# Performance work log

Hardware: AMD Instinct MI355X
Metric: run time of the kernel (lower is better)

## Reference

```python
import jax, jax.numpy as jnp
import numpy as np

B, Q, K, D, H = 4, 2048, 2048, 512, 8
DH = D // H
MASK_VAL = -1e6


def setup_inputs() -> dict:
    key = jax.random.key(0)
    ks = jax.random.split(key, 8)
    queries = jax.random.normal(ks[0], (B, Q, D), dtype=jnp.float32)
    keys = jax.random.normal(ks[1], (B, K, D), dtype=jnp.float32)
    values = jax.random.normal(ks[2], (B, K, D), dtype=jnp.float32)
    valid_lens = jax.random.randint(ks[3], (B,), 1, K + 1, dtype=jnp.int32)
    # torch nn.Linear weights: shape [out_features, in_features], y = x @ W.T
    s = 1.0 / np.sqrt(D)
    W_q = jax.random.uniform(ks[4], (D, D), jnp.float32, -s, s)
    W_k = jax.random.uniform(ks[5], (D, D), jnp.float32, -s, s)
    W_v = jax.random.uniform(ks[6], (D, D), jnp.float32, -s, s)
    W_o = jax.random.uniform(ks[7], (D, D), jnp.float32, -s, s)
    return {"queries": queries, "keys": keys, "values": values,
            "valid_lens": valid_lens, "W_q": W_q, "W_k": W_k,
            "W_v": W_v, "W_o": W_o}


def _split_heads(x):
    # [B, S, D] -> [B, H, S, DH]
    b, s, _ = x.shape
    return x.reshape(b, s, H, DH).transpose(0, 2, 1, 3)


def reference(queries, keys, values, valid_lens, W_q, W_k, W_v, W_o):
    q = _split_heads(queries @ W_q.T)   # [B,H,Q,DH]
    k = _split_heads(keys @ W_k.T)      # [B,H,K,DH]
    v = _split_heads(values @ W_v.T)    # [B,H,K,DH]
    scores = jnp.einsum("bhqd,bhkd->bhqk", q, k) / jnp.sqrt(jnp.float32(DH))
    # padding mask: key position < valid_len[b], broadcast over heads & queries
    mask = jnp.arange(K)[None, None, None, :] < valid_lens[:, None, None, None]
    scores = jnp.where(mask, scores, MASK_VAL)
    attn = jax.nn.softmax(scores, axis=-1)  # dropout=eval/no-op
    out = jnp.einsum("bhqk,bhkd->bhqd", attn, v)
    out = out.transpose(0, 2, 1, 3).reshape(queries.shape[0], q.shape[2], D)
    return out @ W_o.T
```

## Files before the change

kernel.cpp:

```cpp
#include <hip/hip_runtime.h>
#include <cstdint>
#include <cstddef>

#define BB  4
#define QQ  2048
#define SK  2048
#define DD  512
#define HH  8
#define DHH 64
#define SPLIT 4

typedef __bf16 bf16;
typedef bf16  bf16x8 __attribute__((ext_vector_type(8)));
typedef bf16  bf16x4 __attribute__((ext_vector_type(4)));
typedef float f32x4  __attribute__((ext_vector_type(4)));
typedef _Float16 f16;
typedef f16   f16x4 __attribute__((ext_vector_type(4)));
typedef f16   f16x8 __attribute__((ext_vector_type(8)));

__device__ __forceinline__ void async16(void* lds, const void* g) {
  __builtin_amdgcn_global_load_lds(
      (const __attribute__((address_space(1))) unsigned int*)g,
      (__attribute__((address_space(3))) unsigned int*)lds, 16, 0, 0);
}

__global__ __launch_bounds__(256) void cvt_all(
    const float* __restrict__ q, const float* __restrict__ k,
    const float* __restrict__ v, const float* __restrict__ w0,
    const float* __restrict__ w1, const float* __restrict__ w2,
    const float* __restrict__ w3, bf16* __restrict__ dq,
    bf16* __restrict__ dk, bf16* __restrict__ dv, bf16* __restrict__ dw0,
    bf16* __restrict__ dw1, bf16* __restrict__ dw2, bf16* __restrict__ dw3,
    int nx4, int nw4) {
  const int y = blockIdx.y;
  const float* s;
  bf16* d;
  int n4;
  if (y < 3) {
    n4 = nx4; s = y == 0 ? q : y == 1 ? k : v;
    d = y == 0 ? dq : y == 1 ? dk : dv;
  } else {
    n4 = nw4;
    s = y == 3 ? w0 : y == 4 ? w1 : y == 5 ? w2 : w3;
    d = y == 3 ? dw0 : y == 4 ? dw1 : y == 5 ? dw2 : dw3;
  }
  int i = blockIdx.x * 256 + threadIdx.x;
  if (i < n4) {
    float4 vv = ((const float4*)s)[i];
    bf16x4 o;
    o[0] = (bf16)vv.x; o[1] = (bf16)vv.y; o[2] = (bf16)vv.z; o[3] = (bf16)vv.w;
    ((bf16x4*)d)[i] = o;
  }
}

template <typename EpiF>
__device__ __forceinline__ void gemm_body(
    const bf16* __restrict__ A, const bf16* __restrict__ Bt, EpiF epi_fn) {
  __shared__ __align__(16) bf16 lA[2][128 * 64];
  __shared__ __align__(16) bf16 lB[2][64 * 64];
  const int tid  = threadIdx.x;
  const int l    = tid & 63;
  const int w    = tid >> 6;
  const int lrow = l & 15, lq = l >> 4;
  const int wm = (w >> 1) * 64, wn = (w & 1) * 32;
  const int tM = blockIdx.y * 128, tN = blockIdx.x * 64;

  auto stage = [&](int kt, int buf) {
#pragma unroll
    for (int j = 0; j < 4; ++j) {
      int c = j * 256 + tid, row = c >> 3, gcc = (c & 7) ^ (row & 7);
      async16(&lA[buf][c * 8], &A[(size_t)(tM + row) * DD + kt + gcc * 8]);
    }
#pragma unroll
    for (int j = 0; j < 2; ++j) {
      int c = j * 256 + tid, row = c >> 3, gcc = (c & 7) ^ (row & 7);
      async16(&lB[buf][c * 8], &Bt[(size_t)(tN + row) * DD + kt + gcc * 8]);
    }
  };

  f32x4 acc[4][2] = {};
  stage(0, 0);
  for (int it = 0; it < 8; ++it) {
    __syncthreads();
    if (it + 1 < 8) stage((it + 1) * 64, (it + 1) & 1);
    const bf16* bufA = lA[it & 1];
    const bf16* bufB = lB[it & 1];
#pragma unroll
    for (int ks = 0; ks < 2; ++ks) {
      bf16x8 af[4], bfr[2];
#pragma unroll
      for (int mt = 0; mt < 4; ++mt) {
        int row = wm + mt * 16 + lrow;
        int chunk = row * 8 + ((ks * 4 + lq) ^ (lrow & 7));
        af[mt] = *(const bf16x8*)&bufA[chunk * 8];
      }
#pragma unroll
      for (int nt = 0; nt < 2; ++nt) {
        int row = wn + nt * 16 + lrow;
        int chunk = row * 8 + ((ks * 4 + lq) ^ (lrow & 7));
        bfr[nt] = *(const bf16x8*)&bufB[chunk * 8];
      }
#pragma unroll
      for (int mt = 0; mt < 4; ++mt)
#pragma unroll
        for (int nt = 0; nt < 2; ++nt)
          acc[mt][nt] = __builtin_amdgcn_mfma_f32_16x16x32_bf16(
              af[mt], bfr[nt], acc[mt][nt], 0, 0, 0);
    }
  }

#pragma unroll
  for (int mt = 0; mt < 4; ++mt)
#pragma unroll
    for (int nt = 0; nt < 2; ++nt) {
      int gi0 = tM + wm + mt * 16 + lq * 4;
      int gc  = tN + wn + nt * 16 + lrow;
      epi_fn(acc[mt][nt], gi0, gc);
    }
}

__global__ __launch_bounds__(256, 3) void proj3(
    const bf16* __restrict__ xq, const bf16* __restrict__ wq, bf16* __restrict__ qh,
    const bf16* __restrict__ xk, const bf16* __restrict__ wk, bf16* __restrict__ kh,
    const bf16* __restrict__ xv, const bf16* __restrict__ wv, bf16* __restrict__ vt,
    float qscale) {
  const int z = blockIdx.z;
  const bf16* A  = z == 0 ? xq : z == 1 ? xk : xv;
  const bf16* Bt = z == 0 ? wq : z == 1 ? wk : wv;
  bf16* Cout     = z == 0 ? qh : z == 1 ? kh : vt;
  const float scale = z == 0 ? qscale : 1.0f;
  gemm_body(A, Bt, [&](const f32x4& a, int gi0, int gc) {
    if (z == 2) {
      int b2 = gi0 >> 11, s0 = gi0 & 2047;
      int h2 = gc >> 6,  dh = gc & 63;
      int tile = s0 >> 6, kk = s0 & 63;
      int g = kk >> 4, a2 = (kk >> 2) & 3;
      int idx0 = ((g >> 1) * 4 + a2) * 8 + (g & 1) * 4;
      bf16x4 o;
#pragma unroll
      for (int r = 0; r < 4; ++r) o[r] = (bf16)a[r];
      *(bf16x4*)&Cout[((size_t)(b2 * HH + h2) * DHH + dh) * SK + tile * 64 + idx0] = o;
    } else {
#pragma unroll
      for (int r = 0; r < 4; ++r) {
        int gi = gi0 + r;
        int b2 = gi >> 11, s = gi & 2047;
        int h2 = gc >> 6,  dh = gc & 63;
        Cout[((size_t)(b2 * HH + h2) * QQ + s) * DHH + dh] = (bf16)(a[r] * scale);
      }
    }
  });
}

__global__ __launch_bounds__(256, 3) void proj_o(
    const bf16* __restrict__ A, const bf16* __restrict__ Bt,
    float* __restrict__ Cout) {
  gemm_body(A, Bt, [&](const f32x4& a, int gi0, int gc) {
#pragma unroll
    for (int r = 0; r < 4; ++r)
      Cout[(size_t)(gi0 + r) * DD + gc] = a[r];
  });
}

__global__ __launch_bounds__(256, 5) void attn_split(
    const bf16* __restrict__ qh, const bf16* __restrict__ kh,
    const bf16* __restrict__ vt, const int* __restrict__ valid_lens,
    f16* __restrict__ opart, float* __restrict__ lpart) {
  __shared__ __align__(16) bf16 lK[2][64 * 64];
  __shared__ __align__(16) bf16 lV[2][64 * 64];
  const int tid  = threadIdx.x;
  const int l    = tid & 63;
  const int w    = tid >> 6;
  const int lrow = l & 15, lq = l >> 4;
  const int rx   = lrow & 7;
  const int bh = blockIdx.x;
  const int b = bh >> 3;
  const int qt = blockIdx.y, z = blockIdx.z;
  const int vl  = valid_lens[b];
  const int nkt = (vl + 63) >> 6;
  const int chunk = (nkt + SPLIT - 1) / SPLIT;
  const int kt0 = z * chunk;
  const int kt1 = min(nkt, kt0 + chunk);
  const size_t pbase = ((size_t)bh * 32 + qt) * SPLIT + z;
  float* lout = lpart + pbase * 64;
  f16*   oout = opart + pbase * 4096;

  if (kt0 >= kt1) {
    if (lq == 0) lout[w * 16 + lrow] = 0.f;
    return;
  }

  const int q0 = qt * 64 + w * 16;
  const bf16* qbase = qh + (size_t)bh * QQ * DHH;
  const bf16* kbase = kh + (size_t)bh * SK * DHH;
  const bf16* vbase = vt + (size_t)bh * DHH * SK;

  bf16x8 qf[2];
#pragma unroll
  for (int ks = 0; ks < 2; ++ks)
    qf[ks] = *(const bf16x8*)&qbase[(size_t)(q0 + lrow) * DHH + ks * 32 + lq * 8];

  auto stageKV = [&](int k0, int buf) {
#pragma unroll
    for (int j = 0; j < 2; ++j) {
      int c = j * 256 + tid, row = c >> 3, gcc = (c & 7) ^ (row & 7);
      async16(&lK[buf][c * 8], &kbase[(size_t)(k0 + row) * DHH + gcc * 8]);
    }
#pragma unroll
    for (int j = 0; j < 2; ++j) {
      int c = j * 256 + tid, row = c >> 3, gcc = (c & 7) ^ (row & 7);
      async16(&lV[buf][c * 8], &vbase[(size_t)row * SK + k0 + gcc * 8]);
    }
  };

  f32x4 acc[4] = {};
  float rs = 0.f;

  stageKV(kt0 * 64, kt0 & 1);
  for (int kt = kt0; kt < kt1; ++kt) {
    __syncthreads();
    if (kt + 1 < kt1) stageKV((kt + 1) * 64, (kt + 1) & 1);
    const bf16* bufK = lK[kt & 1];
    const bf16* bufV = lV[kt & 1];
    const int k0 = kt * 64;

    f32x4 s[4] = {};
#pragma unroll
    for (int ks = 0; ks < 2; ++ks) {
#pragma unroll
      for (int t = 0; t < 4; ++t) {
        int row = t * 16 + lrow;
        int chunkc = row * 8 + ((ks * 4 + lq) ^ rx);
        bf16x8 kf = *(const bf16x8*)&bufK[chunkc * 8];
        s[t] = __builtin_amdgcn_mfma_f32_16x16x32_bf16(kf, qf[ks], s[t], 0, 0, 0);
      }
    }

    if (vl < k0 + 64) {
#pragma unroll
      for (int t = 0; t < 4; ++t) {
        int kb = k0 + t * 16 + lq * 4;
#pragma unroll
        for (int r = 0; r < 4; ++r)
          if (kb + r >= vl) s[t][r] = -1e30f;
      }
    }

    bf16x4 sb[4];
#pragma unroll
    for (int t = 0; t < 4; ++t)
#pragma unroll
      for (int r = 0; r < 4; ++r) {
        float p = __builtin_amdgcn_exp2f(fminf(s[t][r], 80.f));
        rs += p;
        sb[t][r] = (bf16)p;
      }

#pragma unroll
    for (int p = 0; p < 2; ++p) {
      bf16x8 pb;
#pragma unroll
      for (int r = 0; r < 4; ++r) { pb[r] = sb[2 * p][r]; pb[4 + r] = sb[2 * p + 1][r]; }
      int cc = (p * 4 + lq) ^ rx;
#pragma unroll
      for (int mt = 0; mt < 4; ++mt) {
        int row = mt * 16 + lrow;
        bf16x8 vf = *(const bf16x8*)&bufV[(row * 8 + cc) * 8];
        acc[mt] = __builtin_amdgcn_mfma_f32_16x16x32_bf16(vf, pb, acc[mt], 0, 0, 0);
      }
    }
  }

  rs += __shfl_xor(rs, 16);
  rs += __shfl_xor(rs, 32);
  if (lq == 0) lout[w * 16 + lrow] = rs;

#pragma unroll
  for (int mt = 0; mt < 4; ++mt) {
    f16x4 o;
#pragma unroll
    for (int r = 0; r < 4; ++r) o[r] = (f16)acc[mt][r];
    *(f16x4*)&oout[(w * 16 + lrow) * 64 + mt * 16 + lq * 4] = o;
  }
}

__global__ __launch_bounds__(256) void attn_combine(
    const f16* __restrict__ opart, const float* __restrict__ lpart,
    bf16* __restrict__ ao) {
  const int bh = blockIdx.x, qt = blockIdx.y;
  const int b = bh >> 3, h = bh & 7;
  const size_t base = ((size_t)bh * 32 + qt) * SPLIT;
  const int t = threadIdx.x, q = t >> 2, ds = (t & 3) * 16;
  float O[16] = {};
  float lsum = 0.f;
#pragma unroll
  for (int z = 0; z < SPLIT; ++z) {
    float lz = lpart[(base + z) * 64 + q];
    if (lz != 0.f) {
      lsum += lz;
      const f16x8* p = (const f16x8*)&opart[(base + z) * 4096 + q * 64 + ds];
      f16x8 a = p[0], c = p[1];
#pragma unroll
      for (int r = 0; r < 8; ++r) { O[r] += (float)a[r]; O[8 + r] += (float)c[r]; }
    }
  }
  float inv = 1.0f / lsum;
  bf16x8 o0, o1;
#pragma unroll
  for (int r = 0; r < 8; ++r) {
    o0[r] = (bf16)(O[r] * inv);
    o1[r] = (bf16)(O[8 + r] * inv);
  }
  bf16* dst = &ao[((size_t)(b * QQ + qt * 64 + q)) * DD + h * DHH + ds];
  *(bf16x8*)dst = o0;
  *(bf16x8*)(dst + 8) = o1;
}

extern "C" void kernel_launch(void* const* d_in, const int* in_sizes, int n_in,
                              void* d_out, int out_size, void* d_ws, size_t ws_size,
                              hipStream_t stream) {
  const float* queries    = (const float*)d_in[0];
  const float* keys       = (const float*)d_in[1];
  const float* values     = (const float*)d_in[2];
  const int*   valid_lens = (const int*)d_in[3];
  const float* W_q = (const float*)d_in[4];
  const float* W_k = (const float*)d_in[5];
  const float* W_v = (const float*)d_in[6];
  const float* W_o = (const float*)d_in[7];

  const size_t NX = (size_t)BB * QQ * DD;
  const size_t NW = (size_t)DD * DD;

  bf16* xq = (bf16*)d_ws;
  bf16* xk = xq + NX;
  bf16* xv = xk + NX;
  bf16* wq = xv + NX;
  bf16* wk = wq + NW;
  bf16* wv = wk + NW;
  bf16* wo = wv + NW;
  bf16* qh = wo + NW;
  bf16* kh = qh + NX;
  bf16* vt = kh + NX;
  f16*  opart = (f16*)(vt + NX);
  float* lpart = (float*)(opart + (size_t)32 * 32 * SPLIT * 4096);
  bf16* ao = xq;

  dim3 blk(256);
  cvt_all<<<dim3(NX / 1024, 7), blk, 0, stream>>>(
      queries, keys, values, W_q, W_k, W_v, W_o,
      xq, xk, xv, wq, wk, wv, wo, (int)(NX / 4), (int)(NW / 4));

  const float qscale = 0.125f * 1.44269504088896340736f;
  dim3 gg(DD / 64, (BB * QQ) / 128, 3);
  proj3<<<gg, blk, 0, stream>>>(xq, wq, qh, xk, wk, kh, xv, wv, vt, qscale);

  attn_split<<<dim3(BB * HH, QQ / 64, SPLIT), blk, 0, stream>>>(
      qh, kh, vt, valid_lens, opart, lpart);
  attn_combine<<<dim3(BB * HH, QQ / 64), blk, 0, stream>>>(opart, lpart, ao);

  proj_o<<<dim3(DD / 64, (BB * QQ) / 128), blk, 0, stream>>>(ao, wo, (float*)d_out);
}
```

Before: 202.9 us.

## Enlarge GEMM and attention tiles, fixed key chunks, transposed Q/K/O projections

```diff
diff --git a/kernel.cpp b/kernel.cpp
--- a/kernel.cpp
+++ b/kernel.cpp
@@ -8,7 +8,8 @@
 #define DD  512
 #define HH  8
 #define DHH 64
-#define SPLIT 4
+#define CS  8
+#define ZMAX 4
 
 typedef __bf16 bf16;
 typedef bf16  bf16x8 __attribute__((ext_vector_type(8)));
@@ -22,6 +23,11 @@
   __builtin_amdgcn_global_load_lds(
       (const __attribute__((address_space(1))) unsigned int*)g,
       (__attribute__((address_space(3))) unsigned int*)lds, 16, 0, 0);
+}
+
+__device__ __forceinline__ uint32_t pk2(float lo, float hi) {
+  return __builtin_amdgcn_perm(__builtin_bit_cast(uint32_t, hi),
+                               __builtin_bit_cast(uint32_t, lo), 0x07060302u);
 }
 
 __global__ __launch_bounds__(256) void cvt_all(
@@ -53,32 +59,32 @@
   }
 }
 
-template <typename EpiF>
+template <int MT, typename EpiF>
 __device__ __forceinline__ void gemm_body(
-    const bf16* __restrict__ A, const bf16* __restrict__ Bt, EpiF epi_fn) {
-  __shared__ __align__(16) bf16 lA[2][128 * 64];
-  __shared__ __align__(16) bf16 lB[2][64 * 64];
+    const bf16* __restrict__ A, const bf16* __restrict__ B,
+    int tM, int tN, EpiF epi_fn) {
+  __shared__ __align__(16) bf16 lA[2][MT * 32 * 64];
+  __shared__ __align__(16) bf16 lB[2][128 * 64];
   const int tid  = threadIdx.x;
   const int l    = tid & 63;
   const int w    = tid >> 6;
   const int lrow = l & 15, lq = l >> 4;
-  const int wm = (w >> 1) * 64, wn = (w & 1) * 32;
-  const int tM = blockIdx.y * 128, tN = blockIdx.x * 64;
+  const int wm = (w >> 1) * (MT * 16), wn = (w & 1) * 64;
 
   auto stage = [&](int kt, int buf) {
+#pragma unroll
+    for (int j = 0; j < MT; ++j) {
+      int c = j * 256 + tid, row = c >> 3, gcc = (c & 7) ^ (row & 7);
+      async16(&lA[buf][c * 8], &A[(size_t)(tM + row) * DD + kt + gcc * 8]);
+    }
 #pragma unroll
     for (int j = 0; j < 4; ++j) {
       int c = j * 256 + tid, row = c >> 3, gcc = (c & 7) ^ (row & 7);
-      async16(&lA[buf][c * 8], &A[(size_t)(tM + row) * DD + kt + gcc * 8]);
-    }
-#pragma unroll
-    for (int j = 0; j < 2; ++j) {
-      int c = j * 256 + tid, row = c >> 3, gcc = (c & 7) ^ (row & 7);
-      async16(&lB[buf][c * 8], &Bt[(size_t)(tN + row) * DD + kt + gcc * 8]);
+      async16(&lB[buf][c * 8], &B[(size_t)(tN + row) * DD + kt + gcc * 8]);
     }
   };
 
-  f32x4 acc[4][2] = {};
+  f32x4 acc[MT][4] = {};
   stage(0, 0);
   for (int it = 0; it < 8; ++it) {
     __syncthreads();
@@ -87,82 +93,85 @@
     const bf16* bufB = lB[it & 1];
 #pragma unroll
     for (int ks = 0; ks < 2; ++ks) {
-      bf16x8 af[4], bfr[2];
-#pragma unroll
-      for (int mt = 0; mt < 4; ++mt) {
+      bf16x8 af[MT], bfr[4];
+#pragma unroll
+      for (int mt = 0; mt < MT; ++mt) {
         int row = wm + mt * 16 + lrow;
         int chunk = row * 8 + ((ks * 4 + lq) ^ (lrow & 7));
         af[mt] = *(const bf16x8*)&bufA[chunk * 8];
       }
 #pragma unroll
-      for (int nt = 0; nt < 2; ++nt) {
+      for (int nt = 0; nt < 4; ++nt) {
         int row = wn + nt * 16 + lrow;
         int chunk = row * 8 + ((ks * 4 + lq) ^ (lrow & 7));
         bfr[nt] = *(const bf16x8*)&bufB[chunk * 8];
       }
 #pragma unroll
-      for (int mt = 0; mt < 4; ++mt)
-#pragma unroll
-        for (int nt = 0; nt < 2; ++nt)
+      for (int mt = 0; mt < MT; ++mt)
+#pragma unroll
+        for (int nt = 0; nt < 4; ++nt)
           acc[mt][nt] = __builtin_amdgcn_mfma_f32_16x16x32_bf16(
               af[mt], bfr[nt], acc[mt][nt], 0, 0, 0);
     }
   }
 
 #pragma unroll
-  for (int mt = 0; mt < 4; ++mt)
-#pragma unroll
-    for (int nt = 0; nt < 2; ++nt) {
-      int gi0 = tM + wm + mt * 16 + lq * 4;
-      int gc  = tN + wn + nt * 16 + lrow;
-      epi_fn(acc[mt][nt], gi0, gc);
-    }
-}
-
-__global__ __launch_bounds__(256, 3) void proj3(
+  for (int mt = 0; mt < MT; ++mt)
+#pragma unroll
+    for (int nt = 0; nt < 4; ++nt) {
+      int row0 = tM + wm + mt * 16 + lq * 4;
+      int col  = tN + wn + nt * 16 + lrow;
+      epi_fn(acc[mt][nt], row0, col);
+    }
+}
+
+__global__ __launch_bounds__(256, 2) void proj3(
     const bf16* __restrict__ xq, const bf16* __restrict__ wq, bf16* __restrict__ qh,
     const bf16* __restrict__ xk, const bf16* __restrict__ wk, bf16* __restrict__ kh,
     const bf16* __restrict__ xv, const bf16* __restrict__ wv, bf16* __restrict__ vt,
     float qscale) {
-  const int z = blockIdx.z;
-  const bf16* A  = z == 0 ? xq : z == 1 ? xk : xv;
-  const bf16* Bt = z == 0 ? wq : z == 1 ? wk : wv;
-  bf16* Cout     = z == 0 ? qh : z == 1 ? kh : vt;
-  const float scale = z == 0 ? qscale : 1.0f;
-  gemm_body(A, Bt, [&](const f32x4& a, int gi0, int gc) {
-    if (z == 2) {
-      int b2 = gi0 >> 11, s0 = gi0 & 2047;
-      int h2 = gc >> 6,  dh = gc & 63;
+  const int z = blockIdx.y, x = blockIdx.x;
+  if (z < 2) {
+    const bf16* A  = z == 0 ? wq : wk;
+    const bf16* B  = z == 0 ? xq : xk;
+    bf16* Cout     = z == 0 ? qh : kh;
+    const float scale = z == 0 ? qscale : 1.0f;
+    int tM = (x & 3) * 128, tN = (x >> 2) * 128;
+    gemm_body<4>(A, B, tM, tN, [&](const f32x4& a, int row0, int col) {
+      int b2 = col >> 11, s = col & 2047;
+      int h2 = row0 >> 6, dh0 = row0 & 63;
+      bf16x4 o;
+#pragma unroll
+      for (int r = 0; r < 4; ++r) o[r] = (bf16)(a[r] * scale);
+      *(bf16x4*)&Cout[((size_t)(b2 * HH + h2) * QQ + s) * DHH + dh0] = o;
+    });
+  } else {
+    int tM = (x >> 2) * 128, tN = (x & 3) * 128;
+    gemm_body<4>(xv, wv, tM, tN, [&](const f32x4& a, int row0, int col) {
+      int b2 = row0 >> 11, s0 = row0 & 2047;
+      int h2 = col >> 6,  dh = col & 63;
       int tile = s0 >> 6, kk = s0 & 63;
       int g = kk >> 4, a2 = (kk >> 2) & 3;
       int idx0 = ((g >> 1) * 4 + a2) * 8 + (g & 1) * 4;
       bf16x4 o;
 #pragma unroll
       for (int r = 0; r < 4; ++r) o[r] = (bf16)a[r];
-      *(bf16x4*)&Cout[((size_t)(b2 * HH + h2) * DHH + dh) * SK + tile * 64 + idx0] = o;
-    } else {
-#pragma unroll
-      for (int r = 0; r < 4; ++r) {
-        int gi = gi0 + r;
-        int b2 = gi >> 11, s = gi & 2047;
-        int h2 = gc >> 6,  dh = gc & 63;
-        Cout[((size_t)(b2 * HH + h2) * QQ + s) * DHH + dh] = (bf16)(a[r] * scale);
-      }
-    }
+      *(bf16x4*)&vt[((size_t)(b2 * HH + h2) * DHH + dh) * SK + tile * 64 + idx0] = o;
+    });
+  }
+}
+
+__global__ __launch_bounds__(256, 2) void proj_o(
+    const bf16* __restrict__ wo, const bf16* __restrict__ ao,
+    float* __restrict__ Cout) {
+  const int x = blockIdx.x;
+  int tM = (x & 7) * 64, tN = (x >> 3) * 128;
+  gemm_body<2>(wo, ao, tM, tN, [&](const f32x4& a, int row0, int col) {
+    *(float4*)&Cout[(size_t)col * DD + row0] = *(const float4*)&a;
   });
 }
 
-__global__ __launch_bounds__(256, 3) void proj_o(
-    const bf16* __restrict__ A, const bf16* __restrict__ Bt,
-    float* __restrict__ Cout) {
-  gemm_body(A, Bt, [&](const f32x4& a, int gi0, int gc) {
-#pragma unroll
-    for (int r = 0; r < 4; ++r)
-      Cout[(size_t)(gi0 + r) * DD + gc] = a[r];
-  });
-}
-
-__global__ __launch_bounds__(256, 5) void attn_split(
+__global__ __launch_bounds__(256, 4) void attn_split(
     const bf16* __restrict__ qh, const bf16* __restrict__ kh,
     const bf16* __restrict__ vt, const int* __restrict__ valid_lens,
     f16* __restrict__ opart, float* __restrict__ lpart) {
@@ -178,27 +187,29 @@
   const int qt = blockIdx.y, z = blockIdx.z;
   const int vl  = valid_lens[b];
   const int nkt = (vl + 63) >> 6;
-  const int chunk = (nkt + SPLIT - 1) / SPLIT;
-  const int kt0 = z * chunk;
-  const int kt1 = min(nkt, kt0 + chunk);
-  const size_t pbase = ((size_t)bh * 32 + qt) * SPLIT + z;
-  float* lout = lpart + pbase * 64;
-  f16*   oout = opart + pbase * 4096;
+  const int kt0 = z * CS;
+  const int kt1 = min(nkt, kt0 + CS);
+  const size_t pbase = ((size_t)bh * 16 + qt) * ZMAX + z;
+  float* lout = lpart + pbase * 128;
+  f16*   oout = opart + pbase * 8192;
 
   if (kt0 >= kt1) {
-    if (lq == 0) lout[w * 16 + lrow] = 0.f;
+    if (tid < 128) lout[tid] = 0.f;
     return;
   }
 
-  const int q0 = qt * 64 + w * 16;
+  const int q0 = qt * 128 + w * 32;
   const bf16* qbase = qh + (size_t)bh * QQ * DHH;
   const bf16* kbase = kh + (size_t)bh * SK * DHH;
   const bf16* vbase = vt + (size_t)bh * DHH * SK;
 
-  bf16x8 qf[2];
-#pragma unroll
-  for (int ks = 0; ks < 2; ++ks)
-    qf[ks] = *(const bf16x8*)&qbase[(size_t)(q0 + lrow) * DHH + ks * 32 + lq * 8];
+  bf16x8 qf[2][2];
+#pragma unroll
+  for (int g = 0; g < 2; ++g)
+#pragma unroll
+    for (int ks = 0; ks < 2; ++ks)
+      qf[g][ks] = *(const bf16x8*)
+          &qbase[(size_t)(q0 + g * 16 + lrow) * DHH + ks * 32 + lq * 8];
 
   auto stageKV = [&](int k0, int buf) {
 #pragma unroll
@@ -213,8 +224,8 @@
     }
   };
 
-  f32x4 acc[4] = {};
-  float rs = 0.f;
+  f32x4 acc[2][4] = {};
+  float rs[2] = {0.f, 0.f};
 
   stageKV(kt0 * 64, kt0 & 1);
   for (int kt = kt0; kt < kt1; ++kt) {
@@ -224,7 +235,7 @@
     const bf16* bufV = lV[kt & 1];
     const int k0 = kt * 64;
 
-    f32x4 s[4] = {};
+    f32x4 s[2][4] = {};
 #pragma unroll
     for (int ks = 0; ks < 2; ++ks) {
 #pragma unroll
@@ -232,7 +243,10 @@
         int row = t * 16 + lrow;
         int chunkc = row * 8 + ((ks * 4 + lq) ^ rx);
         bf16x8 kf = *(const bf16x8*)&bufK[chunkc * 8];
-        s[t] = __builtin_amdgcn_mfma_f32_16x16x32_bf16(kf, qf[ks], s[t], 0, 0, 0);
+#pragma unroll
+        for (int g = 0; g < 2; ++g)
+          s[g][t] = __builtin_amdgcn_mfma_f32_16x16x32_bf16(
+              kf, qf[g][ks], s[g][t], 0, 0, 0);
       }
     }
 
@@ -242,46 +256,60 @@
         int kb = k0 + t * 16 + lq * 4;
 #pragma unroll
         for (int r = 0; r < 4; ++r)
-          if (kb + r >= vl) s[t][r] = -1e30f;
-      }
-    }
-
-    bf16x4 sb[4];
-#pragma unroll
-    for (int t = 0; t < 4; ++t)
-#pragma unroll
-      for (int r = 0; r < 4; ++r) {
-        float p = __builtin_amdgcn_exp2f(fminf(s[t][r], 80.f));
-        rs += p;
-        sb[t][r] = (bf16)p;
-      }
-
-#pragma unroll
-    for (int p = 0; p < 2; ++p) {
-      bf16x8 pb;
-#pragma unroll
-      for (int r = 0; r < 4; ++r) { pb[r] = sb[2 * p][r]; pb[4 + r] = sb[2 * p + 1][r]; }
-      int cc = (p * 4 + lq) ^ rx;
+          if (kb + r >= vl) { s[0][t][r] = -1e30f; s[1][t][r] = -1e30f; }
+      }
+    }
+
+#pragma unroll
+    for (int g = 0; g < 2; ++g)
+#pragma unroll
+      for (int t = 0; t < 4; ++t)
+#pragma unroll
+        for (int r = 0; r < 4; ++r) {
+          float p = __builtin_amdgcn_exp2f(s[g][t][r]);
+          rs[g] += p;
+          s[g][t][r] = p;
+        }
+
+#pragma unroll
+    for (int p2 = 0; p2 < 2; ++p2) {
+      union { bf16x8 v; uint32_t u[4]; } pb[2];
+#pragma unroll
+      for (int g = 0; g < 2; ++g) {
+        pb[g].u[0] = pk2(s[g][2 * p2][0], s[g][2 * p2][1]);
+        pb[g].u[1] = pk2(s[g][2 * p2][2], s[g][2 * p2][3]);
+        pb[g].u[2] = pk2(s[g][2 * p2 + 1][0], s[g][2 * p2 + 1][1]);
+        pb[g].u[3] = pk2(s[g][2 * p2 + 1][2], s[g][2 * p2 + 1][3]);
+      }
+      int cc = (p2 * 4 + lq) ^ rx;
 #pragma unroll
       for (int mt = 0; mt < 4; ++mt) {
         int row = mt * 16 + lrow;
         bf16x8 vf = *(const bf16x8*)&bufV[(row * 8 + cc) * 8];
-        acc[mt] = __builtin_amdgcn_mfma_f32_16x16x32_bf16(vf, pb, acc[mt], 0, 0, 0);
-      }
-    }
-  }
-
-  rs += __shfl_xor(rs, 16);
-  rs += __shfl_xor(rs, 32);
-  if (lq == 0) lout[w * 16 + lrow] = rs;
-
-#pragma unroll
-  for (int mt = 0; mt < 4; ++mt) {
-    f16x4 o;
-#pragma unroll
-    for (int r = 0; r < 4; ++r) o[r] = (f16)acc[mt][r];
-    *(f16x4*)&oout[(w * 16 + lrow) * 64 + mt * 16 + lq * 4] = o;
-  }
+#pragma unroll
+        for (int g = 0; g < 2; ++g)
+          acc[g][mt] = __builtin_amdgcn_mfma_f32_16x16x32_bf16(
+              vf, pb[g].v, acc[g][mt], 0, 0, 0);
+      }
+    }
+  }
+
+#pragma unroll
+  for (int g = 0; g < 2; ++g) {
+    rs[g] += __shfl_xor(rs[g], 16);
+    rs[g] += __shfl_xor(rs[g], 32);
+    if (lq == 0) lout[w * 32 + g * 16 + lrow] = rs[g];
+  }
+
+#pragma unroll
+  for (int g = 0; g < 2; ++g)
+#pragma unroll
+    for (int mt = 0; mt < 4; ++mt) {
+      f16x4 o;
+#pragma unroll
+      for (int r = 0; r < 4; ++r) o[r] = (f16)acc[g][mt][r];
+      *(f16x4*)&oout[(w * 32 + g * 16 + lrow) * 64 + mt * 16 + lq * 4] = o;
+    }
 }
 
 __global__ __launch_bounds__(256) void attn_combine(
@@ -289,31 +317,33 @@
     bf16* __restrict__ ao) {
   const int bh = blockIdx.x, qt = blockIdx.y;
   const int b = bh >> 3, h = bh & 7;
-  const size_t base = ((size_t)bh * 32 + qt) * SPLIT;
-  const int t = threadIdx.x, q = t >> 2, ds = (t & 3) * 16;
-  float O[16] = {};
+  const size_t base = ((size_t)bh * 16 + qt) * ZMAX;
+  const int t = threadIdx.x, q = t >> 1, ds = (t & 1) * 32;
+  float O[32] = {};
   float lsum = 0.f;
 #pragma unroll
-  for (int z = 0; z < SPLIT; ++z) {
-    float lz = lpart[(base + z) * 64 + q];
+  for (int z = 0; z < ZMAX; ++z) {
+    float lz = lpart[(base + z) * 128 + q];
     if (lz != 0.f) {
       lsum += lz;
-      const f16x8* p = (const f16x8*)&opart[(base + z) * 4096 + q * 64 + ds];
-      f16x8 a = p[0], c = p[1];
-#pragma unroll
-      for (int r = 0; r < 8; ++r) { O[r] += (float)a[r]; O[8 + r] += (float)c[r]; }
+      const f16x8* p = (const f16x8*)&opart[(base + z) * 8192 + q * 64 + ds];
+#pragma unroll
+      for (int j = 0; j < 4; ++j) {
+        f16x8 a = p[j];
+#pragma unroll
+        for (int r = 0; r < 8; ++r) O[j * 8 + r] += (float)a[r];
+      }
     }
   }
   float inv = 1.0f / lsum;
-  bf16x8 o0, o1;
-#pragma unroll
-  for (int r = 0; r < 8; ++r) {
-    o0[r] = (bf16)(O[r] * inv);
-    o1[r] = (bf16)(O[8 + r] * inv);
-  }
-  bf16* dst = &ao[((size_t)(b * QQ + qt * 64 + q)) * DD + h * DHH + ds];
-  *(bf16x8*)dst = o0;
-  *(bf16x8*)(dst + 8) = o1;
+  bf16* dst = &ao[((size_t)(b * QQ + qt * 128 + q)) * DD + h * DHH + ds];
+#pragma unroll
+  for (int j = 0; j < 4; ++j) {
+    bf16x8 o;
+#pragma unroll
+    for (int r = 0; r < 8; ++r) o[r] = (bf16)(O[j * 8 + r] * inv);
+    *(bf16x8*)(dst + j * 8) = o;
+  }
 }
 
 extern "C" void kernel_launch(void* const* d_in, const int* in_sizes, int n_in,
@@ -342,7 +372,7 @@
   bf16* kh = qh + NX;
   bf16* vt = kh + NX;
   f16*  opart = (f16*)(vt + NX);
-  float* lpart = (float*)(opart + (size_t)32 * 32 * SPLIT * 4096);
+  float* lpart = (float*)(opart + (size_t)32 * 16 * ZMAX * 8192);
   bf16* ao = xq;
 
   dim3 blk(256);
@@ -351,12 +381,12 @@
       xq, xk, xv, wq, wk, wv, wo, (int)(NX / 4), (int)(NW / 4));
 
   const float qscale = 0.125f * 1.44269504088896340736f;
-  dim3 gg(DD / 64, (BB * QQ) / 128, 3);
-  proj3<<<gg, blk, 0, stream>>>(xq, wq, qh, xk, wk, kh, xv, wv, vt, qscale);
-
-  attn_split<<<dim3(BB * HH, QQ / 64, SPLIT), blk, 0, stream>>>(
+  proj3<<<dim3(256, 3), blk, 0, stream>>>(xq, wq, qh, xk, wk, kh, xv, wv, vt,
+                                          qscale);
+
+  attn_split<<<dim3(BB * HH, QQ / 128, ZMAX), blk, 0, stream>>>(
       qh, kh, vt, valid_lens, opart, lpart);
-  attn_combine<<<dim3(BB * HH, QQ / 64), blk, 0, stream>>>(opart, lpart, ao);
-
-  proj_o<<<dim3(DD / 64, (BB * QQ) / 128), blk, 0, stream>>>(ao, wo, (float*)d_out);
-}
+  attn_combine<<<dim3(BB * HH, QQ / 128), blk, 0, stream>>>(opart, lpart, ao);
+
+  proj_o<<<dim3(512), blk, 0, stream>>>(wo, ao, (float*)d_out);
+}
```

Result: faster. 193.9 us (-4.4%).
